# Performance work log

Hardware: AMD Instinct MI355X
Metric: run time of the kernel (lower is better)

The kernel has to match this reference:

```python
import jax, jax.numpy as jnp
import numpy as np

HEADS = 4
NEG_SLOPE = 0.2
LN_EPS = 1e-5


def _layernorm(h, g, b):
    mu = h.mean(-1, keepdims=True)
    var = ((h - mu) ** 2).mean(-1, keepdims=True)
    return (h - mu) / jnp.sqrt(var + LN_EPS) * g + b


def _forward(x, edge_attr, vnf_context,
             w_node, b_node, w_edge_emb, b_edge_emb,
             w_eproj, b_eproj, w_vnf, b_vnf,
             attn_w1, attn_b1, attn_w2, attn_b2, attn_w3, attn_b3,
             gat_w, gat_att_src, gat_att_dst, gat_we, gat_att_e, gat_b,
             ln_g, ln_b,
             venc_w1, venc_b1, venc_w2, venc_b2,
             lstm_wih, lstm_whh, lstm_bih, lstm_bhh,
             out_w1, out_b1, out_w2, out_b2, out_w3, out_b3,
             edge_index):
    N = x.shape[0]
    C = w_node.shape[1]  # hidden_dim = per-head out_channels
    L = gat_w.shape[0]
    src, dst = edge_index[0], edge_index[1]

    # embeddings
    xh = x @ w_node + b_node                        # [N, C]
    ea = edge_attr @ w_edge_emb + b_edge_emb        # [E, C]

    # EdgeAttentionLayer (vnf_context branch, no network_state)
    ef = ea @ w_eproj + b_eproj                     # [E, C]
    vemb = vnf_context @ w_vnf + b_vnf              # [C]
    comb = jnp.concatenate([ef, jnp.broadcast_to(vemb, ef.shape)], axis=-1)
    h1 = jax.nn.relu(comb @ attn_w1 + attn_b1)
    h2 = jax.nn.relu(h1 @ attn_w2 + attn_b2)
    edge_attention = jax.nn.sigmoid(h2 @ attn_w3 + attn_b3)[:, 0]   # [E]
    e_enh = ef * edge_attention[:, None]            # weighted edge features [E, C]

    # PathQualityAwareConv stack: GATConv(heads=4, concat=False, edge_dim=C)
    for l in range(L):
        xr = xh
        xs = (xh @ gat_w[l]).reshape(N, HEADS, C)               # [N, H, C]
        efeat = (e_enh @ gat_we[l]).reshape(-1, HEADS, C)        # [E, H, C]
        a = (jnp.einsum('ehc,hc->eh', xs[src], gat_att_src[l])
             + jnp.einsum('ehc,hc->eh', xs[dst], gat_att_dst[l])
             + jnp.einsum('ehc,hc->eh', efeat, gat_att_e[l]))
        a = jax.nn.leaky_relu(a, NEG_SLOPE)
        amax = jax.ops.segment_max(a, dst, num_segments=N)
        amax = jnp.where(jnp.isfinite(amax), amax, 0.0)
        ae = jnp.exp(a - amax[dst])
        denom = jax.ops.segment_sum(ae, dst, num_segments=N)
        alpha = ae / (denom[dst] + 1e-16)                        # [E, H]
        msg = xs[src] * alpha[:, :, None]                        # [E, H, C]
        agg = jax.ops.segment_sum(msg, dst, num_segments=N)      # [N, H, C]
        h = agg.mean(axis=1) + gat_b[l]                          # concat=False -> head mean
        h = _layernorm(h, ln_g[l], ln_b[l])
        xh = h + xr                                              # residual (same size)

    # vnf context encoder
    v = jax.nn.relu(vnf_context @ venc_w1 + venc_b1) @ venc_w2 + venc_b2  # [C]

    # Set2Set pooling, single graph, processing_steps=3, LSTM(2C -> C)
    hS = jnp.zeros((C,), xh.dtype)
    cS = jnp.zeros((C,), xh.dtype)
    q_star = jnp.zeros((2 * C,), xh.dtype)
    for _ in range(3):
        gates = lstm_wih @ q_star + lstm_bih + lstm_whh @ hS + lstm_bhh
        gi, gf, gg, go = jnp.split(gates, 4)
        cS = jax.nn.sigmoid(gf) * cS + jax.nn.sigmoid(gi) * jnp.tanh(gg)
        hS = jax.nn.sigmoid(go) * jnp.tanh(cS)
        q = hS
        a_sc = jax.nn.softmax(xh @ q)                            # [N]
        r = a_sc @ xh                                            # [C]
        q_star = jnp.concatenate([q, r])

    combined = jnp.concatenate([q_star, v])                      # [3C]
    o = jax.nn.relu(combined @ out_w1 + out_b1)
    o = jax.nn.relu(o @ out_w2 + out_b2)
    o = jax.nn.relu(o @ out_w3 + out_b3)
    return o[None, :]                                            # [1, output_dim]


def setup_inputs() -> dict:
    key = jax.random.key(0)
    ks = jax.random.split(key, 40)
    N, E, C, L = 50000, 200000, 128, 3
    H = HEADS
    rn = lambda k, s, sc=0.05: (jax.random.normal(k, s, jnp.float32) * sc)
    z = lambda *s: jnp.zeros(s, jnp.float32)
    return {
        'x': jax.random.normal(ks[0], (N, 8), jnp.float32),
        'edge_index': jax.random.randint(ks[1], (2, E), 0, N),
        'edge_attr': jax.random.uniform(ks[2], (E, 4), dtype=jnp.float32),
        'vnf_context': jax.random.normal(ks[3], (6,), jnp.float32),
        'w_node': rn(ks[4], (8, C)), 'b_node': z(C),
        'w_edge_emb': rn(ks[5], (4, C)), 'b_edge_emb': z(C),
        'w_eproj': rn(ks[6], (C, C)), 'b_eproj': z(C),
        'w_vnf': rn(ks[7], (6, C)), 'b_vnf': z(C),
        'attn_w1': rn(ks[8], (2 * C, C)), 'attn_b1': z(C),
        'attn_w2': rn(ks[9], (C, C // 2)), 'attn_b2': z(C // 2),
        'attn_w3': rn(ks[10], (C // 2, 1)), 'attn_b3': z(1),
        'gat_w': rn(ks[11], (L, C, H * C)),
        'gat_att_src': rn(ks[12], (L, H, C)),
        'gat_att_dst': rn(ks[13], (L, H, C)),
        'gat_we': rn(ks[14], (L, C, H * C)),
        'gat_att_e': rn(ks[15], (L, H, C)),
        'gat_b': z(L, C),
        'ln_g': jnp.ones((L, C), jnp.float32), 'ln_b': z(L, C),
        'venc_w1': rn(ks[16], (6, C)), 'venc_b1': z(C),
        'venc_w2': rn(ks[17], (C, C)), 'venc_b2': z(C),
        'lstm_wih': rn(ks[18], (4 * C, 2 * C)), 'lstm_whh': rn(ks[19], (4 * C, C)),
        'lstm_bih': z(4 * C), 'lstm_bhh': z(4 * C),
        'out_w1': rn(ks[20], (3 * C, C)), 'out_b1': z(C),
        'out_w2': rn(ks[21], (C, C // 2)), 'out_b2': z(C // 2),
        'out_w3': rn(ks[22], (C // 2, 256)), 'out_b3': z(256),
    }


def reference(x, edge_index, edge_attr, vnf_context,
              w_node, b_node, w_edge_emb, b_edge_emb,
              w_eproj, b_eproj, w_vnf, b_vnf,
              attn_w1, attn_b1, attn_w2, attn_b2, attn_w3, attn_b3,
              gat_w, gat_att_src, gat_att_dst, gat_we, gat_att_e, gat_b,
              ln_g, ln_b,
              venc_w1, venc_b1, venc_w2, venc_b2,
              lstm_wih, lstm_whh, lstm_bih, lstm_bhh,
              out_w1, out_b1, out_w2, out_b2, out_w3, out_b3):
    return _forward(x, edge_attr, vnf_context,
                    w_node, b_node, w_edge_emb, b_edge_emb,
                    w_eproj, b_eproj, w_vnf, b_vnf,
                    attn_w1, attn_b1, attn_w2, attn_b2, attn_w3, attn_b3,
                    gat_w, gat_att_src, gat_att_dst, gat_we, gat_att_e, gat_b,
                    ln_g, ln_b,
                    venc_w1, venc_b1, venc_w2, venc_b2,
                    lstm_wih, lstm_whh, lstm_bih, lstm_bhh,
                    out_w1, out_b1, out_w2, out_b2, out_w3, out_b3,
                    edge_index)
```

## Files before the change

kernel.cpp:

```cpp
#include <hip/hip_runtime.h>
#include <math.h>

#define CC 128
#define HH 4
#define LL 3
#define LNEPS 1e-5f

typedef unsigned int u32;
typedef unsigned short ushort;
typedef float f32x16 __attribute__((ext_vector_type(16)));
typedef __bf16 bf16x8 __attribute__((ext_vector_type(8)));
union Frag { uint4 q; bf16x8 b; };

__device__ __forceinline__ ushort bf16rne(float x){ u32 u=__float_as_uint(x); return (ushort)((u + 0x7FFF + ((u>>16)&1))>>16); }
__device__ __forceinline__ float bf2f(ushort h){ return __uint_as_float(((u32)h)<<16); }


__global__ void k_att_collapse(const float* __restrict__ W, const float* __restrict__ att, float* __restrict__ out){
  int idx = blockIdx.x*blockDim.x + threadIdx.x;
  if(idx >= LL*CC*HH) return;
  int h = idx % HH; int k = (idx/HH)%CC; int l = idx/(HH*CC);
  const float* w = W + ((size_t)(l*CC+k))*(HH*CC) + h*CC;
  const float* a = att + (size_t)(l*HH+h)*CC;
  float s=0.f;
  for(int c=0;c<CC;c++) s += w[c]*a[c];
  out[idx] = s;
}

__global__ void k_We(const float* __restrict__ w_ee, const float* __restrict__ w_ep, float* __restrict__ We){
  int idx = blockIdx.x*blockDim.x + threadIdx.x;
  if(idx >= 4*CC) return;
  int c = idx & (CC-1); int k = idx >> 7;
  float s=0.f;
  for(int m=0;m<CC;m++) s += w_ee[k*CC+m]*w_ep[m*CC+c];
  We[idx]=s;
}

__global__ void k_be_vemb(const float* __restrict__ b_ee, const float* __restrict__ w_ep, const float* __restrict__ b_ep,
                          const float* __restrict__ vnf, const float* __restrict__ w_vnf, const float* __restrict__ b_vnf,
                          float* __restrict__ be, float* __restrict__ vemb){
  int t = threadIdx.x;
  if(t<CC){
    float s=b_ep[t];
    for(int m=0;m<CC;m++) s += b_ee[m]*w_ep[m*CC+t];
    be[t]=s;
  } else if(t<2*CC){
    int c=t-CC;
    float s=b_vnf[c];
    for(int j=0;j<6;j++) s += vnf[j]*w_vnf[j*CC+c];
    vemb[c]=s;
  }
}

__global__ void k_h1eff(const float* __restrict__ We, const float* __restrict__ be, const float* __restrict__ vemb,
                        const float* __restrict__ w1, const float* __restrict__ b1,
                        float* __restrict__ Wh1, float* __restrict__ bh1){
  int idx = blockIdx.x*blockDim.x + threadIdx.x;
  if(idx < 4*CC){
    int c = idx & (CC-1); int k = idx>>7;
    float s=0.f;
    for(int m=0;m<CC;m++) s += We[k*CC+m]*w1[m*CC+c];
    Wh1[idx]=s;
  } else if(idx < 5*CC){
    int c = idx - 4*CC;
    float s=b1[c];
    for(int m=0;m<CC;m++) s += be[m]*w1[m*CC+c];
    for(int j=0;j<CC;j++) s += vemb[j]*w1[(CC+j)*CC+c];
    bh1[c]=s;
  }
}

__global__ void k_aelin(const float* __restrict__ We, const float* __restrict__ be, const float* __restrict__ wattE,
                        float* __restrict__ aelin, float* __restrict__ aebias){
  int t = threadIdx.x;
  if(t<48){
    int l=t>>4, k=(t>>2)&3, h=t&3;
    float s=0.f;
    for(int m=0;m<CC;m++) s += We[k*CC+m]*wattE[(size_t)(l*CC+m)*HH+h];
    aelin[t]=s;
  } else if(t<60){
    int i=t-48; int l=i>>2, h=i&3;
    float s=0.f;
    for(int m=0;m<CC;m++) s += be[m]*wattE[(size_t)(l*CC+m)*HH+h];
    aebias[i]=s;
  }
}

__global__ void k_wsplit(const float* __restrict__ gat_w, ushort* __restrict__ BT){
  int idx = blockIdx.x*blockDim.x + threadIdx.x;
  if(idx >= LL*512*CC) return;
  int l = idx >> 16;
  int r = idx & 65535;
  int hk = r >> 7;
  int c  = r & 127;
  int k = hk & 127, h = hk >> 7;
  float v = gat_w[((size_t)(l*CC + k))*(HH*CC) + h*CC + c] * 0.25f;
  ushort hi = bf16rne(v);
  ushort lo = bf16rne(v - bf2f(hi));
  size_t pos = (size_t)l*131072 + ((size_t)(c>>5)*64 + (hk>>3))*512 + (size_t)((c&31)*16 + (hk&7));
  BT[pos]=hi; BT[pos+8]=lo;
}

__global__ void k_w2split(const float* __restrict__ w2, ushort* __restrict__ W2T){
  int idx = blockIdx.x*blockDim.x + threadIdx.x;
  if(idx >= 128*64) return;
  int k = idx>>6, o = idx&63;
  float v = w2[idx];
  ushort hi = bf16rne(v);
  ushort lo = bf16rne(v - bf2f(hi));
  size_t pos = ((size_t)(o>>5)*16 + (k>>3))*512 + (size_t)((o&31)*16 + (k&7));
  W2T[pos]=hi; W2T[pos+8]=lo;
}

__global__ void k_vvec(const float* __restrict__ vnf, const float* __restrict__ w1, const float* __restrict__ b1,
                       const float* __restrict__ w2, const float* __restrict__ b2, float* __restrict__ v){
  __shared__ float hv[CC];
  int t=threadIdx.x;
  float s=b1[t];
  for(int j=0;j<6;j++) s += vnf[j]*w1[j*CC+t];
  hv[t]=fmaxf(s,0.f);
  __syncthreads();
  float o=b2[t];
  for(int j=0;j<CC;j++) o += hv[j]*w2[j*CC+t];
  v[t]=o;
}

__global__ void k_node_embed(const float* __restrict__ x, const float* __restrict__ w, const float* __restrict__ b,
                             float* __restrict__ xh, int N){
  int idx=blockIdx.x*blockDim.x+threadIdx.x;
  if(idx>=N*CC) return;
  int c=idx&(CC-1); int n=idx>>7;
  const float* xr = x+(size_t)n*8;
  float s=b[c];
  #pragma unroll
  for(int k=0;k<8;k++) s += xr[k]*w[k*CC+c];
  xh[idx]=s;
}

__global__ void k_count(const int* __restrict__ dst, int* __restrict__ counts, int E){
  int e=blockIdx.x*blockDim.x+threadIdx.x;
  if(e<E) atomicAdd(&counts[dst[e]],1);
}

__global__ __launch_bounds__(256) void k_scan_blk(const int* __restrict__ counts, int* __restrict__ offsets,
                                                  int* __restrict__ bsum, int N){
  __shared__ int sv[256];
  int t=threadIdx.x; int i=blockIdx.x*256+t;
  int v = (i<N)? counts[i] : 0;
  sv[t]=v;
  __syncthreads();
  for(int off=1;off<256;off<<=1){
    int add = (t>=off)? sv[t-off]:0;
    __syncthreads();
    sv[t]+=add;
    __syncthreads();
  }
  if(i<N) offsets[i]=sv[t]-v;
  if(t==255) bsum[blockIdx.x]=sv[255];
}

__global__ __launch_bounds__(1024) void k_scan_top(int* __restrict__ bsum, int nb){
  __shared__ int sv[1024];
  int t=threadIdx.x;
  int v = (t<nb)? bsum[t] : 0;
  sv[t]=v;
  __syncthreads();
  for(int off=1;off<1024;off<<=1){
    int add = (t>=off)? sv[t-off]:0;
    __syncthreads();
    sv[t]+=add;
    __syncthreads();
  }
  if(t<nb) bsum[t]=sv[t]-v;
}

__global__ void k_scan_add(int* __restrict__ offsets, const int* __restrict__ bsum, int N, int E){
  int i=blockIdx.x*blockDim.x+threadIdx.x;
  if(i<N) offsets[i]+=bsum[i>>8];
  if(i==0) offsets[N]=E;
}

__global__ void k_fill(const int* __restrict__ dst, const int* __restrict__ offsets, int* __restrict__ cursor,
                       int* __restrict__ elist, int E){
  int e=blockIdx.x*blockDim.x+threadIdx.x;
  if(e<E){ int d=dst[e]; int pos=atomicAdd(&cursor[d],1); elist[offsets[d]+pos]=e; }
}

__global__ __launch_bounds__(128) void k_edge_attn(
    const float* __restrict__ edge_attr,
    const float* __restrict__ Wh1, const float* __restrict__ bh1,
    const ushort* __restrict__ W2T, const float* __restrict__ attn_b2,
    const float* __restrict__ attn_w3, const float* __restrict__ attn_b3,
    const float* __restrict__ aelin, const float* __restrict__ aebias,
    float* __restrict__ a_e, int E)
{
  __shared__ __align__(16) ushort h1f[2][16][32][16];
  __shared__ float s_wh1[640];
  __shared__ float s_ea[64][4];
  __shared__ float s_att[64];
  int t = threadIdx.x;
  int e0 = blockIdx.x*64;
  for(int i=t;i<640;i+=128) s_wh1[i] = (i<512)? Wh1[i] : bh1[i-512];
  if(t<64){
    int e=e0+t;
    float4 v = (e<E)? *(const float4*)&edge_attr[(size_t)e*4] : make_float4(0.f,0.f,0.f,0.f);
    s_ea[t][0]=v.x; s_ea[t][1]=v.y; s_ea[t][2]=v.z; s_ea[t][3]=v.w;
  }
  __syncthreads();
  for(int c=t; c<1024; c+=128){
    int e = c&63, kc = c>>6;
    int et = e>>5, row = e&31;
    float ea0=s_ea[e][0], ea1=s_ea[e][1], ea2=s_ea[e][2], ea3=s_ea[e][3];
    ushort hibuf[8], lobuf[8];
    #pragma unroll
    for(int j=0;j<8;j++){
      int k = kc*8+j;
      float v = s_wh1[512+k] + ea0*s_wh1[k] + ea1*s_wh1[128+k] + ea2*s_wh1[256+k] + ea3*s_wh1[384+k];
      v = fmaxf(v, 0.f);
      ushort hi = bf16rne(v);
      hibuf[j]=hi; lobuf[j]=bf16rne(v - bf2f(hi));
    }
    *(uint4*)&h1f[et][kc][row][0] = *(const uint4*)hibuf;
    *(uint4*)&h1f[et][kc][row][8] = *(const uint4*)lobuf;
  }
  __syncthreads();
  int wave=t>>6, lane=t&63;
  int rlane = lane&31, khalf = lane>>5;
  int et = wave;
  f32x16 acc[2];
  #pragma unroll
  for(int o=0;o<2;o++)
    #pragma unroll
    for(int j=0;j<16;j++) acc[o][j]=0.f;
  for(int ks=0; ks<8; ++ks){
    int kq = ks*2 + khalf;
    Frag ah, al;
    ah.q = *(const uint4*)&h1f[et][kq][rlane][0];
    al.q = *(const uint4*)&h1f[et][kq][rlane][8];
    #pragma unroll
    for(int o=0;o<2;o++){
      size_t bb = ((size_t)(o*16 + kq))*512 + (size_t)(rlane*16);
      Frag bh, bl;
      bh.q = *(const uint4*)(W2T + bb);
      bl.q = *(const uint4*)(W2T + bb + 8);
      acc[o] = __builtin_amdgcn_mfma_f32_32x32x16_bf16(ah.b, bh.b, acc[o], 0,0,0);
      acc[o] = __builtin_amdgcn_mfma_f32_32x32x16_bf16(ah.b, bl.b, acc[o], 0,0,0);
      acc[o] = __builtin_amdgcn_mfma_f32_32x32x16_bf16(al.b, bh.b, acc[o], 0,0,0);
    }
  }
  float b2c0 = attn_b2[rlane], b2c1 = attn_b2[rlane+32];
  float w3c0 = attn_w3[rlane], w3c1 = attn_w3[rlane+32];
  float b3v = attn_b3[0];
  #pragma unroll
  for(int reg=0; reg<16; ++reg){
    float val = fmaxf(acc[0][reg]+b2c0,0.f)*w3c0 + fmaxf(acc[1][reg]+b2c1,0.f)*w3c1;
    #pragma unroll
    for(int off=1; off<32; off<<=1) val += __shfl_xor(val, off);
    int rloc = (reg&3) + 8*(reg>>2) + 4*khalf;
    if(rlane==0) s_att[et*32 + rloc] = 1.f/(1.f+expf(-(val + b3v)));
  }
  __syncthreads();
  if(t<64){
    int e = e0+t;
    if(e<E){
      float att = s_att[t];
      float ea0=s_ea[t][0], ea1=s_ea[t][1], ea2=s_ea[t][2], ea3=s_ea[t][3];
      #pragma unroll
      for(int l=0;l<LL;l++){
        float4 v;
        float* out=(float*)&v;
        #pragma unroll
        for(int h=0;h<4;h++){
          out[h] = att*(ea0*aelin[(l*4+0)*4+h] + ea1*aelin[(l*4+1)*4+h]
                      + ea2*aelin[(l*4+2)*4+h] + ea3*aelin[(l*4+3)*4+h] + aebias[l*4+h]);
        }
        *(float4*)&a_e[((size_t)l*E+e)*4] = v;
      }
    }
  }
}

__global__ __launch_bounds__(256) void k_node_ad(const float* __restrict__ xh, const float* __restrict__ wS, const float* __restrict__ wD,
                          float* __restrict__ asrc, float* __restrict__ adst, int N){
  __shared__ float sx[32*129];
  __shared__ float sw[CC*8];
  int t = threadIdx.x;
  int n0 = blockIdx.x*32;
  for(int i=t;i<512;i+=256){ int k=i>>2, h=i&3; sw[k*8+h]=wS[i]; sw[k*8+4+h]=wD[i]; }
  int lim = (N-n0 < 32 ? N-n0 : 32)*128;
  for(int i=t;i<lim;i+=256){ int nl=i>>7, k=i&127; sx[nl*129+k] = xh[(size_t)n0*128 + i]; }
  __syncthreads();
  int node = t>>3, o = t&7;
  if(n0+node < N){
    const float* xr = sx + node*129;
    float s=0.f;
    #pragma unroll 8
    for(int k=0;k<CC;k++) s += xr[k]*sw[k*8+o];
    ((o<4)? asrc : adst)[(n0+node)*4 + (o&3)] = s;
  }
}

__global__ void k_alpha(const float* __restrict__ asrc, const float* __restrict__ adst,
                        const int* __restrict__ offsets, const int* __restrict__ elist,
                        const int* __restrict__ srcArr, float* __restrict__ ael, int N){
  int idx = blockIdx.x*blockDim.x + threadIdx.x;
  if(idx >= N*4) return;
  int n = idx>>2, h = idx&3;
  int beg = offsets[n], end = offsets[n+1];
  if(beg==end) return;
  float ad = adst[n*4+h];
  float m = -1e30f;
  for(int i=beg;i<end;i++){
    int e = elist[i];
    float a = asrc[srcArr[e]*4+h] + ad + ael[e*4+h];
    a = (a>0.f)? a : 0.2f*a;
    m = fmaxf(m,a);
  }
  float s=0.f;
  for(int i=beg;i<end;i++){
    int e = elist[i];
    float a = asrc[srcArr[e]*4+h] + ad + ael[e*4+h];
    a = (a>0.f)? a : 0.2f*a;
    float ex = expf(a-m);
    s += ex;
    ael[e*4+h] = ex;
  }
  float inv = 1.f/(s+1e-16f);
  for(int i=beg;i<end;i++){
    int e = elist[i];
    ael[e*4+h] *= inv;
  }
}

__global__ __launch_bounds__(256) void k_aggregate(
    const float* __restrict__ xh, const int* __restrict__ srcArr,
    const float* __restrict__ alpha, const int* __restrict__ offsets, const int* __restrict__ elist,
    ushort* __restrict__ AB, int N)
{
  __shared__ __align__(16) ushort sAB[4][64][16];
  int wave = threadIdx.x>>6, lane = threadIdx.x&63;
  int n = blockIdx.x*4+wave;
  float2 ac[4];
  #pragma unroll
  for(int h=0;h<4;h++){ ac[h].x=0.f; ac[h].y=0.f; }
  if(n<N){
    int beg = offsets[n], end = offsets[n+1];
    const float4* al4 = (const float4*)alpha;
    for(int i=beg;i<end;i++){
      int e = elist[i];
      int sr = srcArr[e];
      float4 a = al4[e];
      float2 x = *(const float2*)&xh[(size_t)sr*CC + lane*2];
      ac[0].x += a.x*x.x; ac[0].y += a.x*x.y;
      ac[1].x += a.y*x.x; ac[1].y += a.y*x.y;
      ac[2].x += a.z*x.x; ac[2].y += a.z*x.y;
      ac[3].x += a.w*x.x; ac[3].y += a.w*x.y;
    }
  }
  #pragma unroll
  for(int h=0;h<4;h++){
    ushort h0 = bf16rne(ac[h].x), h1 = bf16rne(ac[h].y);
    u32 hi = (u32)h0 | ((u32)h1<<16);
    u32 lo = (u32)bf16rne(ac[h].x - bf2f(h0)) | ((u32)bf16rne(ac[h].y - bf2f(h1))<<16);
    int hk = h*CC + lane*2;
    int st = hk>>3, off = hk&7;
    *(u32*)&sAB[wave][st][off]   = hi;
    *(u32*)&sAB[wave][st][off+8] = lo;
  }
  __syncthreads();
  int n0 = blockIdx.x*4;
  size_t tilebase = ((size_t)(n0>>5))*32768 + (size_t)((n0&31)*16);
  for(int i=threadIdx.x; i<512; i+=256){
    int st = i>>3, p = i&7;
    uint4 v = *(const uint4*)&sAB[p>>1][st][(p&1)*8];
    *(uint4*)&AB[tilebase + (size_t)st*512 + (size_t)p*8] = v;
  }
}

__global__ __launch_bounds__(128) void k_gemm_ln_mfma(
    const ushort* __restrict__ AB, const ushort* __restrict__ BT,
    const float* __restrict__ bias, const float* __restrict__ lng, const float* __restrict__ lnb,
    float* __restrict__ xh, int N)
{
  int tid = threadIdx.x;
  int w = tid>>6, lane = tid&63;
  int rlane = lane&31, khalf = lane>>5;
  int rb = blockIdx.x*2 + w;
  f32x16 acc[4];
  #pragma unroll
  for(int t=0;t<4;t++)
    #pragma unroll
    for(int j=0;j<16;j++) acc[t][j]=0.f;

  const size_t laneoff = (size_t)(rlane*16);
  for(int ks=0; ks<32; ++ks){
    int kq = ks*2 + khalf;
    size_t base = ((size_t)(rb*64 + kq))*512 + laneoff;
    Frag ah, al;
    ah.q = *(const uint4*)(AB + base);
    al.q = *(const uint4*)(AB + base + 8);
    #pragma unroll
    for(int t=0;t<4;t++){
      size_t bb = ((size_t)(t*64 + kq))*512 + laneoff;
      Frag bh, bl;
      bh.q = *(const uint4*)(BT + bb);
      bl.q = *(const uint4*)(BT + bb + 8);
      acc[t] = __builtin_amdgcn_mfma_f32_32x32x16_bf16(ah.b, bh.b, acc[t], 0,0,0);
      acc[t] = __builtin_amdgcn_mfma_f32_32x32x16_bf16(ah.b, bl.b, acc[t], 0,0,0);
      acc[t] = __builtin_amdgcn_mfma_f32_32x32x16_bf16(al.b, bh.b, acc[t], 0,0,0);
    }
  }
  float bias4[4], g4[4], eb4[4];
  #pragma unroll
  for(int t=0;t<4;t++){ int c=t*32+rlane; bias4[t]=bias[c]; g4[t]=lng[c]; eb4[t]=lnb[c]; }
  #pragma unroll
  for(int reg=0; reg<16; ++reg){
    int rloc = (reg&3) + 8*(reg>>2) + 4*khalf;
    int grow = rb*32 + rloc;
    float x0=acc[0][reg]+bias4[0];
    float x1=acc[1][reg]+bias4[1];
    float x2=acc[2][reg]+bias4[2];
    float x3=acc[3][reg]+bias4[3];
    float s = x0+x1+x2+x3;
    #pragma unroll
    for(int off=1; off<32; off<<=1) s += __shfl_xor(s, off);
    float mu = s*(1.f/CC);
    x0-=mu; x1-=mu; x2-=mu; x3-=mu;
    float q = x0*x0+x1*x1+x2*x2+x3*x3;
    #pragma unroll
    for(int off=1; off<32; off<<=1) q += __shfl_xor(q, off);
    float inv = rsqrtf(q*(1.f/CC)+LNEPS);
    if(grow < N){
      size_t gi = (size_t)grow*CC + rlane;
      xh[gi+ 0]  = x0*inv*g4[0] + eb4[0] + xh[gi+ 0];
      xh[gi+32]  = x1*inv*g4[1] + eb4[1] + xh[gi+32];
      xh[gi+64]  = x2*inv*g4[2] + eb4[2] + xh[gi+64];
      xh[gi+96]  = x3*inv*g4[3] + eb4[3] + xh[gi+96];
    }
  }
}

__global__ __launch_bounds__(512) void k_lstm(const float* __restrict__ wih, const float* __restrict__ whh,
                    const float* __restrict__ bih, const float* __restrict__ bhh,
                    const float* __restrict__ qstar, float* __restrict__ hS, float* __restrict__ cS){
  __shared__ float sq[2*CC];
  __shared__ float sh[CC];
  __shared__ float sg[4*CC];
  int t=threadIdx.x;
  if(t<2*CC) sq[t]=qstar[t];
  else if(t<3*CC) sh[t-2*CC]=hS[t-2*CC];
  __syncthreads();
  float a=bih[t]+bhh[t];
  const float* wr = wih + (size_t)t*2*CC;
  for(int j=0;j<2*CC;j++) a += wr[j]*sq[j];
  const float* hr = whh + (size_t)t*CC;
  for(int j=0;j<CC;j++) a += hr[j]*sh[j];
  sg[t]=a;
  __syncthreads();
  if(t<CC){
    float gi=sg[t], gf=sg[CC+t], gg=sg[2*CC+t], go=sg[3*CC+t];
    float c = 1.f/(1.f+expf(-gf))*cS[t] + 1.f/(1.f+expf(-gi))*tanhf(gg);
    float h = 1.f/(1.f+expf(-go))*tanhf(c);
    cS[t]=c; hS[t]=h;
  }
}

__global__ __launch_bounds__(256) void k_s2s1(const float* __restrict__ xh, const float* __restrict__ q,
                                              float* __restrict__ pm, float* __restrict__ ps,
                                              float* __restrict__ pr, int N){
  int t=threadIdx.x, wave=t>>6, lane=t&63;
  float q0=q[lane], q1=q[lane+64];
  float m=-1e30f, s=0.f, r0=0.f, r1=0.f;
  for(int n=blockIdx.x*4+wave; n<N; n+=gridDim.x*4){
    const float* xr = xh+(size_t)n*CC;
    float x0 = xr[lane], x1 = xr[lane+64];
    float v = x0*q0 + x1*q1;
    #pragma unroll
    for(int o=32;o>=1;o>>=1) v += __shfl_xor(v,o);
    float nm = fmaxf(m,v);
    float f = expf(m-nm), g = expf(v-nm);
    s = s*f + g; r0 = r0*f + g*x0; r1 = r1*f + g*x1;
    m = nm;
  }
  __shared__ float sm[4], ss[4], sr[4][128];
  if(lane==0){ sm[wave]=m; ss[wave]=s; }
  sr[wave][lane]=r0; sr[wave][lane+64]=r1;
  __syncthreads();
  if(t<128){
    float M = fmaxf(fmaxf(sm[0],sm[1]),fmaxf(sm[2],sm[3]));
    float e0=expf(sm[0]-M), e1=expf(sm[1]-M), e2=expf(sm[2]-M), e3=expf(sm[3]-M);
    pr[(size_t)blockIdx.x*128+t] = sr[0][t]*e0 + sr[1][t]*e1 + sr[2][t]*e2 + sr[3][t]*e3;
    if(t==0){ pm[blockIdx.x]=M; ps[blockIdx.x]= ss[0]*e0+ss[1]*e1+ss[2]*e2+ss[3]*e3; }
  }
}

__global__ __launch_bounds__(1024) void k_s2s2(const float* __restrict__ pm, const float* __restrict__ ps,
                                               const float* __restrict__ pr, const float* __restrict__ hS,
                                               float* __restrict__ qstar, int NB){
  __shared__ float sM[256];
  __shared__ float sw[256];
  __shared__ float sS[256];
  __shared__ float srs[8][128];
  int t = threadIdx.x;
  if(t<256) sM[t] = (t<NB)? pm[t] : -1e30f;
  __syncthreads();
  for(int off=128; off>=1; off>>=1){
    if(t<off) sM[t] = fmaxf(sM[t], sM[t+off]);
    __syncthreads();
  }
  float M = sM[0];
  if(t<256){
    float w = (t<NB)? expf(pm[t]-M) : 0.f;
    sw[t] = w;
    sS[t] = (t<NB)? ps[t]*w : 0.f;
  }
  __syncthreads();
  for(int off=128; off>=1; off>>=1){
    if(t<off) sS[t] += sS[t+off];
    __syncthreads();
  }
  float ssum = sS[0];
  int g = t>>7, col = t&127;
  float rs = 0.f;
  for(int b=g; b<NB; b+=8) rs += pr[(size_t)b*128+col]*sw[b];
  srs[g][col] = rs;
  __syncthreads();
  if(t<128){
    float r = srs[0][t]+srs[1][t]+srs[2][t]+srs[3][t]+srs[4][t]+srs[5][t]+srs[6][t]+srs[7][t];
    qstar[t]    = hS[t];
    qstar[CC+t] = r/ssum;
  }
}

__global__ __launch_bounds__(256) void k_out(
  const float* __restrict__ qstar, const float* __restrict__ vvec,
  const float* __restrict__ w1, const float* __restrict__ b1,
  const float* __restrict__ w2, const float* __restrict__ b2,
  const float* __restrict__ w3, const float* __restrict__ b3, float* __restrict__ out)
{
  __shared__ float comb[3*CC];
  __shared__ float o1[CC];
  __shared__ float o2[64];
  int t=threadIdx.x;
  if(t<2*CC) comb[t]=qstar[t];
  if(t<CC) comb[2*CC+t]=vvec[t];
  __syncthreads();
  if(t<CC){
    float a=b1[t];
    for(int j=0;j<3*CC;j++) a += comb[j]*w1[j*CC+t];
    o1[t]=fmaxf(a,0.f);
  }
  __syncthreads();
  if(t<64){
    float a=b2[t];
    for(int j=0;j<CC;j++) a += o1[j]*w2[j*64+t];
    o2[t]=fmaxf(a,0.f);
  }
  __syncthreads();
  {
    float a=b3[t];
    for(int j=0;j<64;j++) a += o2[j]*w3[j*256+t];
    out[t]=fmaxf(a,0.f);
  }
}

extern "C" void kernel_launch(void* const* d_in, const int* in_sizes, int n_in,
                              void* d_out, int out_size, void* d_ws, size_t ws_size,
                              hipStream_t stream){
  (void)n_in; (void)out_size; (void)ws_size;
  const float* x        = (const float*)d_in[0];
  const int*   eidx     = (const int*)  d_in[1];
  const float* edge_attr= (const float*)d_in[2];
  const float* vnf      = (const float*)d_in[3];
  const float* w_node   = (const float*)d_in[4];
  const float* b_node   = (const float*)d_in[5];
  const float* w_ee     = (const float*)d_in[6];
  const float* b_ee     = (const float*)d_in[7];
  const float* w_ep     = (const float*)d_in[8];
  const float* b_ep     = (const float*)d_in[9];
  const float* w_vnf    = (const float*)d_in[10];
  const float* b_vnf    = (const float*)d_in[11];
  const float* attn_w1  = (const float*)d_in[12];
  const float* attn_b1  = (const float*)d_in[13];
  const float* attn_w2  = (const float*)d_in[14];
  const float* attn_b2  = (const float*)d_in[15];
  const float* attn_w3  = (const float*)d_in[16];
  const float* attn_b3  = (const float*)d_in[17];
  const float* gat_w    = (const float*)d_in[18];
  const float* att_src  = (const float*)d_in[19];
  const float* att_dst  = (const float*)d_in[20];
  const float* gat_we   = (const float*)d_in[21];
  const float* att_e    = (const float*)d_in[22];
  const float* gat_b    = (const float*)d_in[23];
  const float* ln_g     = (const float*)d_in[24];
  const float* ln_b     = (const float*)d_in[25];
  const float* venc_w1  = (const float*)d_in[26];
  const float* venc_b1  = (const float*)d_in[27];
  const float* venc_w2  = (const float*)d_in[28];
  const float* venc_b2  = (const float*)d_in[29];
  const float* lstm_wih = (const float*)d_in[30];
  const float* lstm_whh = (const float*)d_in[31];
  const float* lstm_bih = (const float*)d_in[32];
  const float* lstm_bhh = (const float*)d_in[33];
  const float* out_w1   = (const float*)d_in[34];
  const float* out_b1   = (const float*)d_in[35];
  const float* out_w2   = (const float*)d_in[36];
  const float* out_b2   = (const float*)d_in[37];
  const float* out_w3   = (const float*)d_in[38];
  const float* out_b3   = (const float*)d_in[39];

  const int N = in_sizes[0]/8;
  const int E = in_sizes[1]/2;
  const int* srcA = eidx;
  const int* dstA = eidx + E;

  const int Npad = ((N+127)/128)*128;
  const size_t asize = (size_t)Npad*1024;
  const int nb = (N+255)/256;
  const int S2SB = 256;

  char* wp = (char*)d_ws;
  auto alloc = [&](size_t bytes)->void*{ void* p=(void*)wp; wp += (bytes+255)&~(size_t)255; return p; };
  float* xh    = (float*)alloc((size_t)N*CC*4);
  ushort* AB   = (ushort*)alloc(asize*2);
  ushort* BT   = (ushort*)alloc((size_t)LL*131072*2);
  ushort* W2T  = (ushort*)alloc((size_t)16384*2);
  float* a_e   = (float*)alloc((size_t)LL*E*HH*4);
  float* asrc  = (float*)alloc((size_t)N*HH*4);
  float* adst  = (float*)alloc((size_t)N*HH*4);
  int* counts  = (int*)alloc((size_t)N*4);
  int* offsets = (int*)alloc((size_t)(N+1)*4);
  int* cursor  = (int*)alloc((size_t)N*4);
  int* elist   = (int*)alloc((size_t)E*4);
  int* bsum    = (int*)alloc((size_t)nb*4);
  float* wattS = (float*)alloc((size_t)LL*CC*HH*4);
  float* wattD = (float*)alloc((size_t)LL*CC*HH*4);
  float* wattE = (float*)alloc((size_t)LL*CC*HH*4);
  float* We    = (float*)alloc(4*CC*4);
  float* be    = (float*)alloc(CC*4);
  float* vemb  = (float*)alloc(CC*4);
  float* Wh1   = (float*)alloc(4*CC*4);
  float* bh1   = (float*)alloc(CC*4);
  float* aelin = (float*)alloc(48*4);
  float* aebias= (float*)alloc(12*4);
  float* vvec  = (float*)alloc(CC*4);
  float* lbuf  = (float*)alloc(4*CC*4);
  float* hS=lbuf; float* cS=lbuf+CC; float* qstar=lbuf+2*CC;
  float* pm    = (float*)alloc((size_t)S2SB*4);
  float* ps    = (float*)alloc((size_t)S2SB*4);
  float* pr    = (float*)alloc((size_t)S2SB*128*4);

  k_att_collapse<<<6,256,0,stream>>>(gat_w, att_src, wattS);
  k_att_collapse<<<6,256,0,stream>>>(gat_w, att_dst, wattD);
  k_att_collapse<<<6,256,0,stream>>>(gat_we, att_e, wattE);
  k_We<<<2,256,0,stream>>>(w_ee, w_ep, We);
  k_be_vemb<<<1,256,0,stream>>>(b_ee, w_ep, b_ep, vnf, w_vnf, b_vnf, be, vemb);
  k_h1eff<<<3,256,0,stream>>>(We, be, vemb, attn_w1, attn_b1, Wh1, bh1);
  k_aelin<<<1,64,0,stream>>>(We, be, wattE, aelin, aebias);
  k_wsplit<<<(LL*512*CC+255)/256,256,0,stream>>>(gat_w, BT);
  k_w2split<<<(128*64+255)/256,256,0,stream>>>(attn_w2, W2T);
  k_vvec<<<1,CC,0,stream>>>(vnf, venc_w1, venc_b1, venc_w2, venc_b2, vvec);
  k_node_embed<<<(N*CC+255)/256,256,0,stream>>>(x, w_node, b_node, xh, N);

  hipMemsetAsync(counts, 0, (size_t)N*4, stream);
  k_count<<<(E+255)/256,256,0,stream>>>(dstA, counts, E);
  k_scan_blk<<<nb,256,0,stream>>>(counts, offsets, bsum, N);
  k_scan_top<<<1,1024,0,stream>>>(bsum, nb);
  k_scan_add<<<nb,256,0,stream>>>(offsets, bsum, N, E);
  hipMemsetAsync(cursor, 0, (size_t)N*4, stream);
  k_fill<<<(E+255)/256,256,0,stream>>>(dstA, offsets, cursor, elist, E);

  k_edge_attn<<<(E+63)/64,128,0,stream>>>(edge_attr, Wh1, bh1, W2T, attn_b2, attn_w3, attn_b3, aelin, aebias, a_e, E);

  for(int l=0;l<LL;l++){
    float* ael = a_e + (size_t)l*E*HH;
    k_node_ad<<<(N+31)/32,256,0,stream>>>(xh, wattS+(size_t)l*CC*HH, wattD+(size_t)l*CC*HH, asrc, adst, N);
    k_alpha<<<(N*4+255)/256,256,0,stream>>>(asrc, adst, offsets, elist, srcA, ael, N);
    k_aggregate<<<(N+3)/4,256,0,stream>>>(xh, srcA, ael, offsets, elist, AB, N);
    k_gemm_ln_mfma<<<Npad/64,128,0,stream>>>(AB, BT+(size_t)l*131072,
                                             gat_b+(size_t)l*CC, ln_g+(size_t)l*CC, ln_b+(size_t)l*CC, xh, N);
  }

  hipMemsetAsync(lbuf, 0, 4*CC*4, stream);
  for(int it=0; it<3; ++it){
    k_lstm<<<1,512,0,stream>>>(lstm_wih, lstm_whh, lstm_bih, lstm_bhh, qstar, hS, cS);
    k_s2s1<<<S2SB,256,0,stream>>>(xh, hS, pm, ps, pr, N);
    k_s2s2<<<1,1024,0,stream>>>(pm, ps, pr, hS, qstar, S2SB);
  }

  k_out<<<1,256,0,stream>>>(qstar, vvec, out_w1, out_b1, out_w2, out_b2, out_w3, out_b3, (float*)d_out);
}
```

Measured before the change: 779.9 us.

## Fuse neighbor aggregation with MFMA GEMM and LayerNorm via shared memory

Merges the aggregation kernel and the GEMM+LayerNorm kernel into one kernel. Each block aggregates 32 nodes into a shared-memory bf16 hi/lo tile, splits the K dimension across four waves, and reduces the partial MFMA accumulators through shared memory before the LayerNorm epilogue. Because other blocks still read neighbor features, xh is now ping-ponged between two buffers. This removes the global AB round trip and one launch per layer, but cuts the number of blocks, adds a serial cross-wave reduction, and uses 64KB of shared memory per block, which may limit occupancy.

```diff
diff --git a/kernel.cpp b/kernel.cpp
--- a/kernel.cpp
+++ b/kernel.cpp
@@ -332,110 +332,120 @@
   }
 }
 
-__global__ __launch_bounds__(256) void k_aggregate(
-    const float* __restrict__ xh, const int* __restrict__ srcArr,
+__global__ __launch_bounds__(256) void k_agg_gemm(
+    const float* __restrict__ xin, const int* __restrict__ srcArr,
     const float* __restrict__ alpha, const int* __restrict__ offsets, const int* __restrict__ elist,
-    ushort* __restrict__ AB, int N)
+    const ushort* __restrict__ BT,
+    const float* __restrict__ bias, const float* __restrict__ lng, const float* __restrict__ lnb,
+    float* __restrict__ xout, int N)
 {
-  __shared__ __align__(16) ushort sAB[4][64][16];
-  int wave = threadIdx.x>>6, lane = threadIdx.x&63;
-  int n = blockIdx.x*4+wave;
-  float2 ac[4];
-  #pragma unroll
-  for(int h=0;h<4;h++){ ac[h].x=0.f; ac[h].y=0.f; }
-  if(n<N){
-    int beg = offsets[n], end = offsets[n+1];
-    const float4* al4 = (const float4*)alpha;
-    for(int i=beg;i<end;i++){
-      int e = elist[i];
-      int sr = srcArr[e];
-      float4 a = al4[e];
-      float2 x = *(const float2*)&xh[(size_t)sr*CC + lane*2];
-      ac[0].x += a.x*x.x; ac[0].y += a.x*x.y;
-      ac[1].x += a.y*x.x; ac[1].y += a.y*x.y;
-      ac[2].x += a.z*x.x; ac[2].y += a.z*x.y;
-      ac[3].x += a.w*x.x; ac[3].y += a.w*x.y;
+  __shared__ __align__(16) ushort sA[64][32][16];
+  int t = threadIdx.x;
+  int wave = t>>6, lane = t&63;
+  int n0 = blockIdx.x*32;
+  const float4* al4 = (const float4*)alpha;
+  for(int j=0;j<8;j++){
+    int r = wave*8+j;
+    int n = n0 + r;
+    float2 ac[4];
+    #pragma unroll
+    for(int h=0;h<4;h++){ ac[h].x=0.f; ac[h].y=0.f; }
+    if(n<N){
+      int beg = offsets[n], end = offsets[n+1];
+      for(int i=beg;i<end;i++){
+        int e = elist[i];
+        int sr = srcArr[e];
+        float4 a = al4[e];
+        float2 x = *(const float2*)&xin[(size_t)sr*CC + lane*2];
+        ac[0].x += a.x*x.x; ac[0].y += a.x*x.y;
+        ac[1].x += a.y*x.x; ac[1].y += a.y*x.y;
+        ac[2].x += a.z*x.x; ac[2].y += a.z*x.y;
+        ac[3].x += a.w*x.x; ac[3].y += a.w*x.y;
+      }
     }
-  }
-  #pragma unroll
-  for(int h=0;h<4;h++){
-    ushort h0 = bf16rne(ac[h].x), h1 = bf16rne(ac[h].y);
-    u32 hi = (u32)h0 | ((u32)h1<<16);
-    u32 lo = (u32)bf16rne(ac[h].x - bf2f(h0)) | ((u32)bf16rne(ac[h].y - bf2f(h1))<<16);
-    int hk = h*CC + lane*2;
-    int st = hk>>3, off = hk&7;
-    *(u32*)&sAB[wave][st][off]   = hi;
-    *(u32*)&sAB[wave][st][off+8] = lo;
-  }
-  __syncthreads();
-  int n0 = blockIdx.x*4;
-  size_t tilebase = ((size_t)(n0>>5))*32768 + (size_t)((n0&31)*16);
-  for(int i=threadIdx.x; i<512; i+=256){
-    int st = i>>3, p = i&7;
-    uint4 v = *(const uint4*)&sAB[p>>1][st][(p&1)*8];
-    *(uint4*)&AB[tilebase + (size_t)st*512 + (size_t)p*8] = v;
-  }
-}
-
-__global__ __launch_bounds__(128) void k_gemm_ln_mfma(
-    const ushort* __restrict__ AB, const ushort* __restrict__ BT,
-    const float* __restrict__ bias, const float* __restrict__ lng, const float* __restrict__ lnb,
-    float* __restrict__ xh, int N)
-{
-  int tid = threadIdx.x;
-  int w = tid>>6, lane = tid&63;
+    #pragma unroll
+    for(int h=0;h<4;h++){
+      ushort h0 = bf16rne(ac[h].x), h1 = bf16rne(ac[h].y);
+      u32 hi = (u32)h0 | ((u32)h1<<16);
+      u32 lo = (u32)bf16rne(ac[h].x - bf2f(h0)) | ((u32)bf16rne(ac[h].y - bf2f(h1))<<16);
+      int hk = h*CC + lane*2;
+      int kq = hk>>3, off = hk&7;
+      *(u32*)&sA[kq][r][off]   = hi;
+      *(u32*)&sA[kq][r][off+8] = lo;
+    }
+  }
+  __syncthreads();
   int rlane = lane&31, khalf = lane>>5;
-  int rb = blockIdx.x*2 + w;
   f32x16 acc[4];
   #pragma unroll
-  for(int t=0;t<4;t++)
-    #pragma unroll
-    for(int j=0;j<16;j++) acc[t][j]=0.f;
-
-  const size_t laneoff = (size_t)(rlane*16);
-  for(int ks=0; ks<32; ++ks){
-    int kq = ks*2 + khalf;
-    size_t base = ((size_t)(rb*64 + kq))*512 + laneoff;
+  for(int t4=0;t4<4;t4++)
+    #pragma unroll
+    for(int j=0;j<16;j++) acc[t4][j]=0.f;
+  for(int ks=0; ks<8; ++ks){
+    int kq = wave*16 + ks*2 + khalf;
     Frag ah, al;
-    ah.q = *(const uint4*)(AB + base);
-    al.q = *(const uint4*)(AB + base + 8);
-    #pragma unroll
-    for(int t=0;t<4;t++){
-      size_t bb = ((size_t)(t*64 + kq))*512 + laneoff;
+    ah.q = *(const uint4*)&sA[kq][rlane][0];
+    al.q = *(const uint4*)&sA[kq][rlane][8];
+    #pragma unroll
+    for(int t4=0;t4<4;t4++){
+      size_t bb = ((size_t)(t4*64 + kq))*512 + (size_t)(rlane*16);
       Frag bh, bl;
       bh.q = *(const uint4*)(BT + bb);
       bl.q = *(const uint4*)(BT + bb + 8);
-      acc[t] = __builtin_amdgcn_mfma_f32_32x32x16_bf16(ah.b, bh.b, acc[t], 0,0,0);
-      acc[t] = __builtin_amdgcn_mfma_f32_32x32x16_bf16(ah.b, bl.b, acc[t], 0,0,0);
-      acc[t] = __builtin_amdgcn_mfma_f32_32x32x16_bf16(al.b, bh.b, acc[t], 0,0,0);
+      acc[t4] = __builtin_amdgcn_mfma_f32_32x32x16_bf16(ah.b, bh.b, acc[t4], 0,0,0);
+      acc[t4] = __builtin_amdgcn_mfma_f32_32x32x16_bf16(ah.b, bl.b, acc[t4], 0,0,0);
+      acc[t4] = __builtin_amdgcn_mfma_f32_32x32x16_bf16(al.b, bh.b, acc[t4], 0,0,0);
     }
   }
-  float bias4[4], g4[4], eb4[4];
-  #pragma unroll
-  for(int t=0;t<4;t++){ int c=t*32+rlane; bias4[t]=bias[c]; g4[t]=lng[c]; eb4[t]=lnb[c]; }
-  #pragma unroll
-  for(int reg=0; reg<16; ++reg){
-    int rloc = (reg&3) + 8*(reg>>2) + 4*khalf;
-    int grow = rb*32 + rloc;
-    float x0=acc[0][reg]+bias4[0];
-    float x1=acc[1][reg]+bias4[1];
-    float x2=acc[2][reg]+bias4[2];
-    float x3=acc[3][reg]+bias4[3];
-    float s = x0+x1+x2+x3;
-    #pragma unroll
-    for(int off=1; off<32; off<<=1) s += __shfl_xor(s, off);
-    float mu = s*(1.f/CC);
-    x0-=mu; x1-=mu; x2-=mu; x3-=mu;
-    float q = x0*x0+x1*x1+x2*x2+x3*x3;
-    #pragma unroll
-    for(int off=1; off<32; off<<=1) q += __shfl_xor(q, off);
-    float inv = rsqrtf(q*(1.f/CC)+LNEPS);
-    if(grow < N){
-      size_t gi = (size_t)grow*CC + rlane;
-      xh[gi+ 0]  = x0*inv*g4[0] + eb4[0] + xh[gi+ 0];
-      xh[gi+32]  = x1*inv*g4[1] + eb4[1] + xh[gi+32];
-      xh[gi+64]  = x2*inv*g4[2] + eb4[2] + xh[gi+64];
-      xh[gi+96]  = x3*inv*g4[3] + eb4[3] + xh[gi+96];
+  __syncthreads();
+  if(wave>0){
+    float* so = ((float*)sA) + (size_t)(wave-1)*4096;
+    #pragma unroll
+    for(int t4=0;t4<4;t4++)
+      #pragma unroll
+      for(int reg=0;reg<16;reg++){
+        int rloc = (reg&3) + 8*(reg>>2) + 4*khalf;
+        so[rloc*128 + t4*32 + rlane] = acc[t4][reg];
+      }
+  }
+  __syncthreads();
+  if(wave==0){
+    const float* s0 = (const float*)sA;
+    #pragma unroll
+    for(int t4=0;t4<4;t4++)
+      #pragma unroll
+      for(int reg=0;reg<16;reg++){
+        int rloc = (reg&3) + 8*(reg>>2) + 4*khalf;
+        int idx = rloc*128 + t4*32 + rlane;
+        acc[t4][reg] += s0[idx] + s0[4096+idx] + s0[8192+idx];
+      }
+    float bias4[4], g4[4], eb4[4];
+    #pragma unroll
+    for(int t4=0;t4<4;t4++){ int c=t4*32+rlane; bias4[t4]=bias[c]; g4[t4]=lng[c]; eb4[t4]=lnb[c]; }
+    #pragma unroll
+    for(int reg=0; reg<16; ++reg){
+      int rloc = (reg&3) + 8*(reg>>2) + 4*khalf;
+      int grow = n0 + rloc;
+      float x0=acc[0][reg]+bias4[0];
+      float x1=acc[1][reg]+bias4[1];
+      float x2=acc[2][reg]+bias4[2];
+      float x3=acc[3][reg]+bias4[3];
+      float s = x0+x1+x2+x3;
+      #pragma unroll
+      for(int off=1; off<32; off<<=1) s += __shfl_xor(s, off);
+      float mu = s*(1.f/CC);
+      x0-=mu; x1-=mu; x2-=mu; x3-=mu;
+      float q = x0*x0+x1*x1+x2*x2+x3*x3;
+      #pragma unroll
+      for(int off=1; off<32; off<<=1) q += __shfl_xor(q, off);
+      float inv = rsqrtf(q*(1.f/CC)+LNEPS);
+      if(grow < N){
+        size_t gi = (size_t)grow*CC + rlane;
+        xout[gi+ 0]  = x0*inv*g4[0] + eb4[0] + xin[gi+ 0];
+        xout[gi+32]  = x1*inv*g4[1] + eb4[1] + xin[gi+32];
+        xout[gi+64]  = x2*inv*g4[2] + eb4[2] + xin[gi+64];
+        xout[gi+96]  = x3*inv*g4[3] + eb4[3] + xin[gi+96];
+      }
     }
   }
 }
@@ -614,15 +624,13 @@
   const int* srcA = eidx;
   const int* dstA = eidx + E;
 
-  const int Npad = ((N+127)/128)*128;
-  const size_t asize = (size_t)Npad*1024;
   const int nb = (N+255)/256;
   const int S2SB = 256;
 
   char* wp = (char*)d_ws;
   auto alloc = [&](size_t bytes)->void*{ void* p=(void*)wp; wp += (bytes+255)&~(size_t)255; return p; };
-  float* xh    = (float*)alloc((size_t)N*CC*4);
-  ushort* AB   = (ushort*)alloc(asize*2);
+  float* xhA   = (float*)alloc((size_t)N*CC*4);
+  float* xhB   = (float*)alloc((size_t)N*CC*4);
   ushort* BT   = (ushort*)alloc((size_t)LL*131072*2);
   ushort* W2T  = (ushort*)alloc((size_t)16384*2);
   float* a_e   = (float*)alloc((size_t)LL*E*HH*4);
@@ -660,7 +668,7 @@
   k_wsplit<<<(LL*512*CC+255)/256,256,0,stream>>>(gat_w, BT);
   k_w2split<<<(128*64+255)/256,256,0,stream>>>(attn_w2, W2T);
   k_vvec<<<1,CC,0,stream>>>(vnf, venc_w1, venc_b1, venc_w2, venc_b2, vvec);
-  k_node_embed<<<(N*CC+255)/256,256,0,stream>>>(x, w_node, b_node, xh, N);
+  k_node_embed<<<(N*CC+255)/256,256,0,stream>>>(x, w_node, b_node, xhA, N);
 
   hipMemsetAsync(counts, 0, (size_t)N*4, stream);
   k_count<<<(E+255)/256,256,0,stream>>>(dstA, counts, E);
@@ -672,19 +680,23 @@
 
   k_edge_attn<<<(E+63)/64,128,0,stream>>>(edge_attr, Wh1, bh1, W2T, attn_b2, attn_w3, attn_b3, aelin, aebias, a_e, E);
 
+  float* cur = xhA;
+  float* nxt = xhB;
   for(int l=0;l<LL;l++){
     float* ael = a_e + (size_t)l*E*HH;
-    k_node_ad<<<(N+31)/32,256,0,stream>>>(xh, wattS+(size_t)l*CC*HH, wattD+(size_t)l*CC*HH, asrc, adst, N);
+    k_node_ad<<<(N+31)/32,256,0,stream>>>(cur, wattS+(size_t)l*CC*HH, wattD+(size_t)l*CC*HH, asrc, adst, N);
     k_alpha<<<(N*4+255)/256,256,0,stream>>>(asrc, adst, offsets, elist, srcA, ael, N);
-    k_aggregate<<<(N+3)/4,256,0,stream>>>(xh, srcA, ael, offsets, elist, AB, N);
-    k_gemm_ln_mfma<<<Npad/64,128,0,stream>>>(AB, BT+(size_t)l*131072,
-                                             gat_b+(size_t)l*CC, ln_g+(size_t)l*CC, ln_b+(size_t)l*CC, xh, N);
+    k_agg_gemm<<<(N+31)/32,256,0,stream>>>(cur, srcA, ael, offsets, elist,
+                                           BT+(size_t)l*131072,
+                                           gat_b+(size_t)l*CC, ln_g+(size_t)l*CC, ln_b+(size_t)l*CC,
+                                           nxt, N);
+    float* tmp = cur; cur = nxt; nxt = tmp;
   }
 
   hipMemsetAsync(lbuf, 0, 4*CC*4, stream);
   for(int it=0; it<3; ++it){
     k_lstm<<<1,512,0,stream>>>(lstm_wih, lstm_whh, lstm_bih, lstm_bhh, qstar, hS, cS);
-    k_s2s1<<<S2SB,256,0,stream>>>(xh, hS, pm, ps, pr, N);
+    k_s2s1<<<S2SB,256,0,stream>>>(cur, hS, pm, ps, pr, N);
     k_s2s2<<<1,1024,0,stream>>>(pm, ps, pr, hS, qstar, S2SB);
   }
 
```

New measurement: 1.396 ms. 79.0% more time.

## Split GEMM K-loop across wave pairs with shared-memory reduction before LayerNorm

Applied to the files above, without the earlier changes.

The node GEMM+LayerNorm kernel now uses 256 threads per block, so each 32-row tile is computed by two waves that each handle half of the K dimension. The second wave writes its partial accumulators to shared memory, and after a barrier the first wave adds them and runs bias, LayerNorm and the residual update. This doubles the number of waves working on the latency-bound MFMA loop to improve latency hiding. The cost is 32KB of LDS per block, one block-wide sync, and an epilogue run by only half the waves.

```diff
diff --git a/kernel.cpp b/kernel.cpp
--- a/kernel.cpp
+++ b/kernel.cpp
@@ -377,15 +377,17 @@
   }
 }
 
-__global__ __launch_bounds__(128) void k_gemm_ln_mfma(
+__global__ __launch_bounds__(256) void k_gemm_ln_mfma(
     const ushort* __restrict__ AB, const ushort* __restrict__ BT,
     const float* __restrict__ bias, const float* __restrict__ lng, const float* __restrict__ lnb,
     float* __restrict__ xh, int N)
 {
+  __shared__ float sred[2][4096];
   int tid = threadIdx.x;
-  int w = tid>>6, lane = tid&63;
+  int wave = tid>>6, lane = tid&63;
+  int pair = wave>>1, p = wave&1;
   int rlane = lane&31, khalf = lane>>5;
-  int rb = blockIdx.x*2 + w;
+  int rb = blockIdx.x*2 + pair;
   f32x16 acc[4];
   #pragma unroll
   for(int t=0;t<4;t++)
@@ -393,8 +395,8 @@
     for(int j=0;j<16;j++) acc[t][j]=0.f;
 
   const size_t laneoff = (size_t)(rlane*16);
-  for(int ks=0; ks<32; ++ks){
-    int kq = ks*2 + khalf;
+  for(int ks=0; ks<16; ++ks){
+    int kq = p*32 + ks*2 + khalf;
     size_t base = ((size_t)(rb*64 + kq))*512 + laneoff;
     Frag ah, al;
     ah.q = *(const uint4*)(AB + base);
@@ -410,32 +412,46 @@
       acc[t] = __builtin_amdgcn_mfma_f32_32x32x16_bf16(al.b, bh.b, acc[t], 0,0,0);
     }
   }
-  float bias4[4], g4[4], eb4[4];
-  #pragma unroll
-  for(int t=0;t<4;t++){ int c=t*32+rlane; bias4[t]=bias[c]; g4[t]=lng[c]; eb4[t]=lnb[c]; }
-  #pragma unroll
-  for(int reg=0; reg<16; ++reg){
-    int rloc = (reg&3) + 8*(reg>>2) + 4*khalf;
-    int grow = rb*32 + rloc;
-    float x0=acc[0][reg]+bias4[0];
-    float x1=acc[1][reg]+bias4[1];
-    float x2=acc[2][reg]+bias4[2];
-    float x3=acc[3][reg]+bias4[3];
-    float s = x0+x1+x2+x3;
-    #pragma unroll
-    for(int off=1; off<32; off<<=1) s += __shfl_xor(s, off);
-    float mu = s*(1.f/CC);
-    x0-=mu; x1-=mu; x2-=mu; x3-=mu;
-    float q = x0*x0+x1*x1+x2*x2+x3*x3;
-    #pragma unroll
-    for(int off=1; off<32; off<<=1) q += __shfl_xor(q, off);
-    float inv = rsqrtf(q*(1.f/CC)+LNEPS);
-    if(grow < N){
-      size_t gi = (size_t)grow*CC + rlane;
-      xh[gi+ 0]  = x0*inv*g4[0] + eb4[0] + xh[gi+ 0];
-      xh[gi+32]  = x1*inv*g4[1] + eb4[1] + xh[gi+32];
-      xh[gi+64]  = x2*inv*g4[2] + eb4[2] + xh[gi+64];
-      xh[gi+96]  = x3*inv*g4[3] + eb4[3] + xh[gi+96];
+  if(p==1){
+    float* so = sred[pair];
+    #pragma unroll
+    for(int t=0;t<4;t++)
+      #pragma unroll
+      for(int reg=0;reg<16;reg++){
+        int rloc = (reg&3) + 8*(reg>>2) + 4*khalf;
+        so[rloc*128 + t*32 + rlane] = acc[t][reg];
+      }
+  }
+  __syncthreads();
+  if(p==0){
+    const float* so = sred[pair];
+    float bias4[4], g4[4], eb4[4];
+    #pragma unroll
+    for(int t=0;t<4;t++){ int c=t*32+rlane; bias4[t]=bias[c]; g4[t]=lng[c]; eb4[t]=lnb[c]; }
+    #pragma unroll
+    for(int reg=0; reg<16; ++reg){
+      int rloc = (reg&3) + 8*(reg>>2) + 4*khalf;
+      int grow = rb*32 + rloc;
+      float x0=acc[0][reg]+so[rloc*128+  0+rlane]+bias4[0];
+      float x1=acc[1][reg]+so[rloc*128+ 32+rlane]+bias4[1];
+      float x2=acc[2][reg]+so[rloc*128+ 64+rlane]+bias4[2];
+      float x3=acc[3][reg]+so[rloc*128+ 96+rlane]+bias4[3];
+      float s = x0+x1+x2+x3;
+      #pragma unroll
+      for(int off=1; off<32; off<<=1) s += __shfl_xor(s, off);
+      float mu = s*(1.f/CC);
+      x0-=mu; x1-=mu; x2-=mu; x3-=mu;
+      float q = x0*x0+x1*x1+x2*x2+x3*x3;
+      #pragma unroll
+      for(int off=1; off<32; off<<=1) q += __shfl_xor(q, off);
+      float inv = rsqrtf(q*(1.f/CC)+LNEPS);
+      if(grow < N){
+        size_t gi = (size_t)grow*CC + rlane;
+        xh[gi+ 0]  = x0*inv*g4[0] + eb4[0] + xh[gi+ 0];
+        xh[gi+32]  = x1*inv*g4[1] + eb4[1] + xh[gi+32];
+        xh[gi+64]  = x2*inv*g4[2] + eb4[2] + xh[gi+64];
+        xh[gi+96]  = x3*inv*g4[3] + eb4[3] + xh[gi+96];
+      }
     }
   }
 }
@@ -677,7 +693,7 @@
     k_node_ad<<<(N+31)/32,256,0,stream>>>(xh, wattS+(size_t)l*CC*HH, wattD+(size_t)l*CC*HH, asrc, adst, N);
     k_alpha<<<(N*4+255)/256,256,0,stream>>>(asrc, adst, offsets, elist, srcA, ael, N);
     k_aggregate<<<(N+3)/4,256,0,stream>>>(xh, srcA, ael, offsets, elist, AB, N);
-    k_gemm_ln_mfma<<<Npad/64,128,0,stream>>>(AB, BT+(size_t)l*131072,
+    k_gemm_ln_mfma<<<Npad/64,256,0,stream>>>(AB, BT+(size_t)l*131072,
                                              gat_b+(size_t)l*CC, ln_g+(size_t)l*CC, ln_b+(size_t)l*CC, xh, N);
   }
 
```

Measured after the change: 780.4 us. Within noise of the previous version (+0.1%).
